# Kernel optimization log

Hardware: AMD Instinct MI355X
Metric: run time of the kernel (lower is better)

Reference implementation:

```python
import jax, jax.numpy as jnp
import numpy as np
from jax import lax

B, C, P = 512, 1, 64
N_MEM = 32768
HID = 16


def _conv(x, w, b):
    # x: [B,Cin,H,W], w: [Cout,Cin,3,3]
    y = lax.conv_general_dilated(x, w, (1, 1), 'SAME',
                                 dimension_numbers=('NCHW', 'OIHW', 'NCHW'))
    return y + b[None, :, None, None]


def setup_inputs() -> dict:
    key = jax.random.key(0)
    ks = jax.random.split(key, 16)
    s = 0.05
    inp = {
        'noisy': jax.random.normal(ks[0], (B, C, P, P), jnp.float32),
        'mem_noise_bank': jax.random.normal(ks[1], (N_MEM, C, P, P), jnp.float32),
        'mem_clean_bank': jax.random.normal(ks[2], (N_MEM, C, P, P), jnp.float32),
        # frozen base denoiser (3-layer residual conv)
        'bw1': jax.random.normal(ks[3], (HID, C, 3, 3), jnp.float32) * s,
        'bb1': jnp.zeros((HID,), jnp.float32),
        'bw2': jax.random.normal(ks[4], (HID, HID, 3, 3), jnp.float32) * s,
        'bb2': jnp.zeros((HID,), jnp.float32),
        'bw3': jax.random.normal(ks[5], (C, HID, 3, 3), jnp.float32) * s,
        'bb3': jnp.zeros((C,), jnp.float32),
        # adapter convs (3*C -> HID -> HID -> C); torch zero-inits last conv,
        # we use small random weights so the output exercises the full path
        'aw1': jax.random.normal(ks[6], (HID, 3 * C, 3, 3), jnp.float32) * s,
        'ab1': jnp.zeros((HID,), jnp.float32),
        'aw2': jax.random.normal(ks[7], (HID, HID, 3, 3), jnp.float32) * s,
        'ab2': jnp.zeros((HID,), jnp.float32),
        'aw3': jax.random.normal(ks[8], (C, HID, 3, 3), jnp.float32) * s,
        'ab3': jnp.zeros((C,), jnp.float32),
    }
    return inp


def _base(noisy, bw1, bb1, bw2, bb2, bw3, bb3):
    h = jax.nn.relu(_conv(noisy, bw1, bb1))
    h = jax.nn.relu(_conv(h, bw2, bb2))
    return noisy - _conv(h, bw3, bb3)


def _select_memory(noisy, mem_noise_bank, mem_clean_bank):
    nf = noisy.reshape(B, -1)                  # [B, D]
    mf = mem_noise_bank.reshape(N_MEM, -1)     # [N, D]
    a2 = jnp.sum(nf * nf, axis=1, keepdims=True)   # [B,1]
    b2 = jnp.sum(mf * mf, axis=1)[None, :]         # [1,N]
    dists = a2 + b2 - 2.0 * (nf @ mf.T)            # [B,N]
    idx = jnp.argmin(dists, axis=1)                # [B]
    return mem_clean_bank[idx]                     # [B,C,P,P]


def reference(noisy, mem_noise_bank, mem_clean_bank,
              bw1, bb1, bw2, bb2, bw3, bb3,
              aw1, ab1, aw2, ab2, aw3, ab3):
    base_out = lax.stop_gradient(_base(noisy, bw1, bb1, bw2, bb2, bw3, bb3))
    mem_clean = lax.stop_gradient(
        _select_memory(noisy, mem_noise_bank, mem_clean_bank))
    x = jnp.concatenate([noisy, base_out, mem_clean], axis=1)  # [B,3C,P,P]
    h = jax.nn.relu(_conv(x, aw1, ab1))
    h = jax.nn.relu(_conv(h, aw2, ab2))
    delta = _conv(h, aw3, ab3)
    return base_out + delta
```

## Files before the change

kernel.cpp:

```cpp
#include <hip/hip_runtime.h>
#include <hip/hip_bf16.h>
#include <cstdint>

#define B_IMG 512
#define NMEM  32768
#define DD    4096
#define HID   16

typedef __attribute__((ext_vector_type(8))) short short8;
typedef __attribute__((ext_vector_type(4))) float f32x4;
typedef unsigned long long ull;

__device__ __forceinline__ void gload16(const void* g, const void* l) {
  __builtin_amdgcn_global_load_lds(
      (const __attribute__((address_space(1))) void*)g,
      (__attribute__((address_space(3))) void*)l, 16, 0, 0);
}

__device__ __forceinline__ ushort to_bf16u(float f) {
  uint32_t u = __float_as_uint(f);
  return (ushort)((u + 0x7fffu + ((u >> 16) & 1u)) >> 16);
}

__device__ __forceinline__ uint32_t cvtpk(float lo, float hi) {
  uint32_t r;
  asm("v_cvt_pk_bf16_f32 %0, %1, %2" : "=v"(r) : "v"(lo), "v"(hi));
  return r;
}

__global__ __launch_bounds__(256) void sqnorm_kernel(const float* __restrict__ x,
                                                     float* __restrict__ out) {
  const int row = blockIdx.x;
  const float4* p = reinterpret_cast<const float4*>(x + (size_t)row * DD);
  float s = 0.f;
#pragma unroll
  for (int j = 0; j < 4; ++j) {
    float4 v = p[threadIdx.x + 256 * j];
    s += v.x * v.x + v.y * v.y + v.z * v.z + v.w * v.w;
  }
#pragma unroll
  for (int o = 32; o > 0; o >>= 1) s += __shfl_down(s, o);
  __shared__ float ls[4];
  if ((threadIdx.x & 63) == 0) ls[threadIdx.x >> 6] = s;
  __syncthreads();
  if (threadIdx.x == 0) out[row] = (ls[0] + ls[1]) + (ls[2] + ls[3]);
}

__global__ __launch_bounds__(256) void split_hi_kernel(const float* __restrict__ x,
                                                       ushort* __restrict__ hi,
                                                       float* __restrict__ nrm) {
  const int row = blockIdx.x;
  const int t = threadIdx.x;
  const float4* p = reinterpret_cast<const float4*>(x + (size_t)row * DD);
  ushort4* ph = reinterpret_cast<ushort4*>(hi + (size_t)row * DD);
  float s = 0.f;
#pragma unroll
  for (int j = 0; j < 4; ++j) {
    float4 v = p[t + 256 * j];
    float vv[4] = {v.x, v.y, v.z, v.w};
    ushort4 h;
    ushort* hp = &h.x;
#pragma unroll
    for (int q = 0; q < 4; ++q) {
      float f = vv[q];
      s += f * f;
      hp[q] = to_bf16u(f);
    }
    ph[t + 256 * j] = h;
  }
#pragma unroll
  for (int o = 32; o > 0; o >>= 1) s += __shfl_down(s, o);
  __shared__ float ls[4];
  if ((t & 63) == 0) ls[t >> 6] = s;
  __syncthreads();
  if (t == 0) nrm[row] = (ls[0] + ls[1]) + (ls[2] + ls[3]);
}

__global__ __launch_bounds__(512) void dist1f_kernel(
    const ushort* __restrict__ Ah_g, const float* __restrict__ Bf,
    const float* __restrict__ a2, float* __restrict__ dists) {
  const int d = blockIdx.x;
  const int xcd = d & 7;
  const int rest = d >> 3;
  const int mb = rest & 3;
  const int nb = (rest >> 2) * 8 + xcd;
  const int m0 = mb * 128;
  const int n0 = nb * 128;

  __shared__ __align__(16) char la[16384];
  __shared__ __align__(16) char lbB[16384];
  __shared__ float b2loc[128];

  const int t = threadIdx.x;
  const int lane = t & 63;
  const int wid = t >> 6;
  const int wm = wid >> 2;
  const int wn = wid & 3;

  f32x4 acc[4][2];
#pragma unroll
  for (int mi = 0; mi < 4; ++mi)
#pragma unroll
    for (int ni = 0; ni < 2; ++ni) {
      f32x4 z = {0.f, 0.f, 0.f, 0.f};
      acc[mi][ni] = z;
    }

  const int r0 = t >> 2, g0 = t & 3;
  const int c0 = ((g0 ^ ((r0 >> 1) & 3)) << 3);
  const float* Bp0 = Bf + (size_t)(n0 + r0) * DD + c0;
  float s0 = 0.f;

  const int arow = t >> 2;
  const int acol = ((g0 ^ ((arow >> 1) & 3)) << 3);

  for (int k0 = 0; k0 < DD; k0 += 64) {
#pragma unroll
    for (int h = 0; h < 2; ++h)
      gload16(Ah_g + ((size_t)(m0 + arow) * DD + k0 + h * 32 + acol),
              la + h * 8192 + t * 16);
#pragma unroll
    for (int h = 0; h < 2; ++h) {
      float4 f00 = *(const float4*)(Bp0 + k0 + h * 32);
      float4 f01 = *(const float4*)(Bp0 + k0 + h * 32 + 4);
      s0 += f00.x * f00.x + f00.y * f00.y + f00.z * f00.z + f00.w * f00.w;
      s0 += f01.x * f01.x + f01.y * f01.y + f01.z * f01.z + f01.w * f01.w;
      uint4 p0;
      p0.x = cvtpk(f00.x, f00.y); p0.y = cvtpk(f00.z, f00.w);
      p0.z = cvtpk(f01.x, f01.y); p0.w = cvtpk(f01.z, f01.w);
      *(uint4*)(lbB + h * 8192 + t * 16) = p0;
    }
    __syncthreads();

#pragma unroll
    for (int h = 0; h < 2; ++h) {
      short8 ah[4];
#pragma unroll
      for (int mi = 0; mi < 4; ++mi) {
        const int r = wm * 64 + mi * 16 + (lane & 15);
        const int off = r * 64 + ((((lane >> 4) ^ (r >> 1)) & 3) << 4);
        ah[mi] = *(const short8*)(la + h * 8192 + off);
      }
#pragma unroll
      for (int ni = 0; ni < 2; ++ni) {
        const int r = wn * 32 + ni * 16 + (lane & 15);
        const int off = r * 64 + ((((lane >> 4) ^ (r >> 1)) & 3) << 4);
        short8 bh = *(const short8*)(lbB + h * 8192 + off);
#pragma unroll
        for (int mi = 0; mi < 4; ++mi)
          acc[mi][ni] = __builtin_amdgcn_mfma_f32_16x16x32_bf16(ah[mi], bh, acc[mi][ni], 0, 0, 0);
      }
    }
    __syncthreads();
  }

  s0 += __shfl_xor(s0, 1); s0 += __shfl_xor(s0, 2);
  if ((t & 3) == 0) b2loc[r0] = s0;
  __syncthreads();

#pragma unroll
  for (int mi = 0; mi < 4; ++mi)
#pragma unroll
    for (int j = 0; j < 4; ++j) {
      const int m = m0 + wm * 64 + mi * 16 + (lane >> 4) * 4 + j;
      const float a2v = a2[m];
#pragma unroll
      for (int ni = 0; ni < 2; ++ni) {
        const int nl = wn * 32 + ni * 16 + (lane & 15);
        dists[(size_t)m * NMEM + n0 + nl] = (a2v + b2loc[nl]) - 2.0f * acc[mi][ni][j];
      }
    }
}

#define MARGIN 4.0f
#define MAXC 64
#define NCH 4
#define CHW (NMEM / NCH)
__global__ __launch_bounds__(256) void refine_kernel(
    const float* __restrict__ dists, const float* __restrict__ A,
    const float* __restrict__ Bm, const float* __restrict__ a2,
    ull* __restrict__ best) {
  const int m = blockIdx.x;
  const int base = blockIdx.y * CHW;
  const int t = threadIdx.x;
  const int lane = t & 63, wid = t >> 6;
  const float4* r4 = reinterpret_cast<const float4*>(dists + (size_t)m * NMEM + base);

  float lmin = 3.4e38f;
  for (int i = t; i < CHW / 4; i += 256) {
    float4 v = r4[i];
    lmin = fminf(lmin, fminf(fminf(v.x, v.y), fminf(v.z, v.w)));
  }
#pragma unroll
  for (int o = 32; o > 0; o >>= 1) lmin = fminf(lmin, __shfl_down(lmin, o));
  __shared__ float ws4[4];
  __shared__ float red[4];
  __shared__ float red2[4];
  __shared__ int cnt;
  __shared__ int cand[MAXC];
  if (lane == 0) ws4[wid] = lmin;
  if (t == 0) cnt = 0;
  __syncthreads();
  const float thresh = fminf(fminf(ws4[0], ws4[1]), fminf(ws4[2], ws4[3])) + MARGIN;

  for (int i = t; i < CHW / 4; i += 256) {
    float4 v = r4[i];
    float vv[4] = {v.x, v.y, v.z, v.w};
#pragma unroll
    for (int q = 0; q < 4; ++q)
      if (vv[q] < thresh) {
        int c = atomicAdd(&cnt, 1);
        if (c < MAXC) cand[c] = base + i * 4 + q;
      }
  }
  __syncthreads();
  const int nc = min(cnt, MAXC);

  ull bkey = ~0ull;
  const float4* a4 = reinterpret_cast<const float4*>(A + (size_t)m * DD);
  for (int c = 0; c < nc; ++c) {
    const int n = cand[c];
    const float4* b4 = reinterpret_cast<const float4*>(Bm + (size_t)n * DD);
    float s = 0.f, s2 = 0.f;
    for (int i = t; i < DD / 4; i += 256) {
      float4 av = a4[i], bv = b4[i];
      s += av.x * bv.x + av.y * bv.y + av.z * bv.z + av.w * bv.w;
      s2 += bv.x * bv.x + bv.y * bv.y + bv.z * bv.z + bv.w * bv.w;
    }
#pragma unroll
    for (int o = 32; o > 0; o >>= 1) {
      s += __shfl_down(s, o);
      s2 += __shfl_down(s2, o);
    }
    if (lane == 0) { red[wid] = s; red2[wid] = s2; }
    __syncthreads();
    if (t == 0) {
      const float dot = (red[0] + red[1]) + (red[2] + red[3]);
      const float b2n = (red2[0] + red2[1]) + (red2[2] + red2[3]);
      const float dv = (a2[m] + b2n) - 2.0f * dot;
      const ull key = ((ull)__float_as_uint(dv) << 32) | (unsigned)n;
      if (key < bkey) bkey = key;
    }
    __syncthreads();
  }
  if (t == 0) atomicMin(&best[m], bkey);
}

__global__ __launch_bounds__(256) void dist_argmin_kernel(
    const float* __restrict__ A, const float* __restrict__ Bm,
    const float* __restrict__ a2, const float* __restrict__ b2,
    ull* __restrict__ best) {
  __shared__ float As[32][128];
  __shared__ float Bs[32][128];
  const int tid = threadIdx.x;
  const int m0 = blockIdx.y * 128;
  const int n0 = blockIdx.x * 128;
  const int tm = tid >> 4, tn = tid & 15;
  const int sr = tid >> 3;
  const int sc = (tid & 7) << 2;
  float acc[8][8];
#pragma unroll
  for (int i = 0; i < 8; ++i)
#pragma unroll
    for (int j = 0; j < 8; ++j) acc[i][j] = 0.f;
  for (int k0 = 0; k0 < DD; k0 += 32) {
    __syncthreads();
#pragma unroll
    for (int r = 0; r < 4; ++r) {
      const int row = sr + (r << 5);
      float4 va = *reinterpret_cast<const float4*>(&A[(size_t)(m0 + row) * DD + k0 + sc]);
      As[sc + 0][row] = va.x; As[sc + 1][row] = va.y;
      As[sc + 2][row] = va.z; As[sc + 3][row] = va.w;
      float4 vb = *reinterpret_cast<const float4*>(&Bm[(size_t)(n0 + row) * DD + k0 + sc]);
      Bs[sc + 0][row] = vb.x; Bs[sc + 1][row] = vb.y;
      Bs[sc + 2][row] = vb.z; Bs[sc + 3][row] = vb.w;
    }
    __syncthreads();
#pragma unroll 8
    for (int kk = 0; kk < 32; ++kk) {
      float4 a0 = *reinterpret_cast<const float4*>(&As[kk][tm * 8]);
      float4 a1 = *reinterpret_cast<const float4*>(&As[kk][tm * 8 + 4]);
      float4 b0 = *reinterpret_cast<const float4*>(&Bs[kk][tn * 8]);
      float4 b1 = *reinterpret_cast<const float4*>(&Bs[kk][tn * 8 + 4]);
      float a[8] = {a0.x, a0.y, a0.z, a0.w, a1.x, a1.y, a1.z, a1.w};
      float b[8] = {b0.x, b0.y, b0.z, b0.w, b1.x, b1.y, b1.z, b1.w};
#pragma unroll
      for (int i = 0; i < 8; ++i)
#pragma unroll
        for (int j = 0; j < 8; ++j) acc[i][j] += a[i] * b[j];
    }
  }
  __syncthreads();
  ull* red = reinterpret_cast<ull*>(&As[0][0]);
#pragma unroll
  for (int i = 0; i < 8; ++i) {
    const int m = m0 + tm * 8 + i;
    const float a2v = a2[m];
    float bd = 3.4e38f;
    int bn = 0;
#pragma unroll
    for (int j = 0; j < 8; ++j) {
      const int n = n0 + tn * 8 + j;
      const float dval = (a2v + b2[n]) - 2.0f * acc[i][j];
      if (dval < bd) { bd = dval; bn = n; }
    }
    red[(tm * 8 + i) * 16 + tn] = ((ull)__float_as_uint(bd) << 32) | (unsigned)bn;
  }
  __syncthreads();
  if (tid < 128) {
    ull k = red[tid * 16];
#pragma unroll
    for (int t2 = 1; t2 < 16; ++t2) {
      ull c = red[tid * 16 + t2];
      if (c < k) k = c;
    }
    atomicMin(&best[m0 + tid], k);
  }
}

__global__ __launch_bounds__(256) void wprep_kernel(
    const float* __restrict__ w1, const float* __restrict__ w2,
    const float* __restrict__ w3, int ncin,
    ushort* __restrict__ wh1, ushort* __restrict__ wl1,
    ushort* __restrict__ wh2, ushort* __restrict__ wl2,
    ushort* __restrict__ wh3, ushort* __restrict__ wl3) {
  const int i = blockIdx.x * 256 + threadIdx.x;
  if (i < 512) {
    const int co = i >> 5, k = i & 31;
    float f = 0.f;
    if (k < ncin * 9) f = w1[(co * ncin + k / 9) * 9 + (k % 9)];
    const ushort hb = to_bf16u(f);
    const float fl = f - __uint_as_float((uint32_t)hb << 16);
    wh1[i] = hb;
    wl1[i] = to_bf16u(fl);
  } else if (i < 512 + 5120) {
    const int j = i - 512;
    const int which = j / 2560;
    const int jj = j % 2560;
    const int co = jj / 160, k = jj % 160;
    float f = 0.f;
    if (which == 0) {
      if (k < 144) f = w2[co * 144 + (k & 15) * 9 + (k >> 4)];
    } else {
      if (co == 0 && k < 144) f = w3[(k & 15) * 9 + (k >> 4)];
    }
    const ushort hb = to_bf16u(f);
    const float fl = f - __uint_as_float((uint32_t)hb << 16);
    ushort* dh = (which == 0) ? wh2 : wh3;
    ushort* dl = (which == 0) ? wl2 : wl3;
    dh[co * 160 + k] = hb;
    dl[co * 160 + k] = to_bf16u(fl);
  }
}

template <int NCIN>
__global__ __launch_bounds__(256, 4) void fused_conv3_kernel(
    const float* __restrict__ chan0, const float* __restrict__ chan1,
    const float* __restrict__ memC, const ull* __restrict__ best,
    const ushort* __restrict__ wh1, const ushort* __restrict__ wl1,
    const float* __restrict__ b1v,
    const ushort* __restrict__ wh2, const ushort* __restrict__ wl2,
    const float* __restrict__ b2v,
    const ushort* __restrict__ wh3, const ushort* __restrict__ wl3,
    const float* __restrict__ b3v,
    const float* __restrict__ addend, float sign, float* __restrict__ outp) {
  constexpr int SIN_SZ = NCIN * 1600;
  constexpr int H1 = SIN_SZ;
  constexpr int H2 = H1 + 10368;
  constexpr int ZP = H2 + 10368;
  constexpr int SB = ZP + 64;
  __shared__ __align__(16) char smem[SB + 128];
  float* sIn = (float*)smem;
  float* sB = (float*)(smem + SB);

  const int tid = threadIdx.x;
  const int lane = tid & 63, wid = tid >> 6;
  const int img = blockIdx.x / 25;
  const int t = blockIdx.x % 25;
  const int y0 = (t / 5) * 14, x0 = (t % 5) * 14;

  const float* cptr[NCIN];
  cptr[0] = chan0 + (size_t)img * DD;
  if (NCIN == 3) {
    cptr[1] = chan1 + (size_t)img * DD;
    cptr[2] = memC + (size_t)(unsigned)(best[img] & 0xffffffffull) * DD;
  }

  if (tid < 16) *(float*)(smem + ZP + tid * 4) = 0.f;
  if (tid < 16) sB[tid] = b1v[tid];
  else if (tid < 32) sB[tid] = b2v[tid - 16];
  for (int i = tid; i < NCIN * 400; i += 256) {
    const int ci = i / 400, r = i % 400, yy = r / 20, xx = r % 20;
    const int gy = y0 + yy - 3, gx = x0 + xx - 3;
    float v = 0.f;
    if (gy >= 0 && gy < 64 && gx >= 0 && gx < 64) v = cptr[ci][gy * 64 + gx];
    sIn[ci * 400 + yy * 20 + xx] = v;
  }
  __syncthreads();

  {
    const int xn15 = lane & 15;
    const int kb = (lane >> 4) * 8;
    const short8 a_hi = *(const short8*)(wh1 + xn15 * 32 + kb);
    const short8 a_lo = *(const short8*)(wl1 + xn15 * 32 + kb);
    int koff[8];
    bool kval[8];
#pragma unroll
    for (int e = 0; e < 8; ++e) {
      const int k = kb + e;
      kval[e] = (k < NCIN * 9);
      const int ci = k / 9, kk = k % 9;
      koff[e] = ci * 400 + (kk / 3) * 20 + (kk % 3);
    }
    for (int g = wid; g < 21; g += 4) {
      const int pxl = g * 16 + xn15;
      const bool pv = (pxl < 324);
      const int py = pxl / 18, pxx = pxl % 18;
      const int pbase = py * 20 + pxx;
      float v[8];
#pragma unroll
      for (int e = 0; e < 8; ++e)
        v[e] = (kval[e] && pv) ? sIn[pbase + koff[e]] : 0.f;
      uint4 bu;
      bu.x = cvtpk(v[0], v[1]); bu.y = cvtpk(v[2], v[3]);
      bu.z = cvtpk(v[4], v[5]); bu.w = cvtpk(v[6], v[7]);
      short8 b = *reinterpret_cast<short8*>(&bu);
      f32x4 z = {0.f, 0.f, 0.f, 0.f};
      f32x4 a1 = __builtin_amdgcn_mfma_f32_16x16x32_bf16(a_lo, b, z, 0, 0, 0);
      a1 = __builtin_amdgcn_mfma_f32_16x16x32_bf16(a_hi, b, a1, 0, 0, 0);
      const int gy = y0 + py - 2, gx = x0 + pxx - 2;
      const bool inimg = pv && ((unsigned)gy < 64u) && ((unsigned)gx < 64u);
      if (pv) {
#pragma unroll
        for (int j = 0; j < 4; ++j) {
          const int co = (lane >> 4) * 4 + j;
          const float val = inimg ? fmaxf(a1[j] + sB[co], 0.f) : 0.f;
          *(ushort*)(smem + H1 + (co >> 3) * 5184 + pxl * 16 + (co & 7) * 2) =
              to_bf16u(val);
        }
      }
    }
  }
  __syncthreads();

  const int xn = lane & 15;
  const int xk = lane >> 4;
  f32x4 acc2[4];
#pragma unroll
  for (int g = 0; g < 4; ++g) { f32x4 z = {0.f, 0.f, 0.f, 0.f}; acc2[g] = z; }
#pragma unroll
  for (int kq = 0; kq < 5; ++kq) {
    const int k0 = kq * 32;
    const int we = xn * 160 + k0 + xk * 8;
    short8 ah = *(const short8*)(wh2 + we);
    short8 al = *(const short8*)(wl2 + we);
    const int kb = k0 + xk * 8;
    const int tap = kb >> 4, cih = (kb >> 3) & 1;
    const bool zp = (tap >= 9);
    const int dy = tap / 3, dx = tap % 3;
    const int bbase = H1 + cih * 5184 + ((dy * 18) + xn + dx) * 16;
#pragma unroll
    for (int g = 0; g < 4; ++g) {
      const int y = wid * 4 + g;
      const int boff = zp ? ZP : (bbase + y * 288);
      short8 b = *(const short8*)(smem + boff);
      acc2[g] = __builtin_amdgcn_mfma_f32_16x16x32_bf16(ah, b, acc2[g], 0, 0, 0);
      acc2[g] = __builtin_amdgcn_mfma_f32_16x16x32_bf16(al, b, acc2[g], 0, 0, 0);
    }
  }
#pragma unroll
  for (int g = 0; g < 4; ++g) {
    const int y = wid * 4 + g;
    const int gy = y0 + y - 1, gx = x0 + xn - 1;
    const bool inimg = ((unsigned)gy < 64u) && ((unsigned)gx < 64u);
#pragma unroll
    for (int j = 0; j < 4; ++j) {
      const int co = xk * 4 + j;
      const float v = inimg ? fmaxf(acc2[g][j] + sB[16 + co], 0.f) : 0.f;
      *(ushort*)(smem + H2 + (co >> 3) * 5184 + (y * 18 + xn) * 16 + (co & 7) * 2) =
          to_bf16u(v);
    }
  }
  __syncthreads();

  f32x4 acc3[4];
#pragma unroll
  for (int g = 0; g < 4; ++g) { f32x4 z = {0.f, 0.f, 0.f, 0.f}; acc3[g] = z; }
#pragma unroll
  for (int kq = 0; kq < 5; ++kq) {
    const int k0 = kq * 32;
    const int we = xn * 160 + k0 + xk * 8;
    short8 ah = *(const short8*)(wh3 + we);
    short8 al = *(const short8*)(wl3 + we);
    const int kb = k0 + xk * 8;
    const int tap = kb >> 4, cih = (kb >> 3) & 1;
    const bool zp = (tap >= 9);
    const int dy = tap / 3, dx = tap % 3;
    const int bbase = H2 + cih * 5184 + ((dy * 18) + xn + dx) * 16;
#pragma unroll
    for (int g = 0; g < 4; ++g) {
      const int y = wid * 4 + g;
      const int boff = zp ? ZP : (bbase + y * 288);
      short8 b = *(const short8*)(smem + boff);
      acc3[g] = __builtin_amdgcn_mfma_f32_16x16x32_bf16(ah, b, acc3[g], 0, 0, 0);
      acc3[g] = __builtin_amdgcn_mfma_f32_16x16x32_bf16(al, b, acc3[g], 0, 0, 0);
    }
  }
  if (xk == 0) {
#pragma unroll
    for (int g = 0; g < 4; ++g) {
      const int y = wid * 4 + g;
      const int gy = y0 + y, gx = x0 + xn;
      if (y < 14 && xn < 14 && gy < 64 && gx < 64) {
        const size_t o = (size_t)img * DD + gy * 64 + gx;
        outp[o] = addend[o] + sign * (acc3[g][0] + b3v[0]);
      }
    }
  }
}

extern "C" void kernel_launch(void* const* d_in, const int* in_sizes, int n_in,
                              void* d_out, int out_size, void* d_ws, size_t ws_size,
                              hipStream_t stream) {
  (void)in_sizes; (void)n_in; (void)out_size;
  const float* noisy = (const float*)d_in[0];
  const float* memN  = (const float*)d_in[1];
  const float* memC  = (const float*)d_in[2];
  const float* bw1 = (const float*)d_in[3];
  const float* bb1 = (const float*)d_in[4];
  const float* bw2 = (const float*)d_in[5];
  const float* bb2 = (const float*)d_in[6];
  const float* bw3 = (const float*)d_in[7];
  const float* bb3 = (const float*)d_in[8];
  const float* aw1 = (const float*)d_in[9];
  const float* ab1 = (const float*)d_in[10];
  const float* aw2 = (const float*)d_in[11];
  const float* ab2 = (const float*)d_in[12];
  const float* aw3 = (const float*)d_in[13];
  const float* ab3 = (const float*)d_in[14];
  float* out_f32 = (float*)d_out;

  char* ws = (char*)d_ws;
  size_t off = 0;
  auto take = [&](size_t bytes) -> char* {
    char* p = ws + off;
    off += (bytes + 255) & ~(size_t)255;
    return p;
  };
  float* b2 = (float*)take((size_t)NMEM * 4);
  float* a2 = (float*)take((size_t)B_IMG * 4);
  ull* best = (ull*)take((size_t)B_IMG * 8);
  float* base_out = (float*)take((size_t)B_IMG * DD * 4);
  ushort* wh1b = (ushort*)take(512 * 2);
  ushort* wl1b = (ushort*)take(512 * 2);
  ushort* wh2b = (ushort*)take(2560 * 2);
  ushort* wl2b = (ushort*)take(2560 * 2);
  ushort* wh3b = (ushort*)take(2560 * 2);
  ushort* wl3b = (ushort*)take(2560 * 2);
  ushort* wh1a = (ushort*)take(512 * 2);
  ushort* wl1a = (ushort*)take(512 * 2);
  ushort* wh2a = (ushort*)take(2560 * 2);
  ushort* wl2a = (ushort*)take(2560 * 2);
  ushort* wh3a = (ushort*)take(2560 * 2);
  ushort* wl3a = (ushort*)take(2560 * 2);
  const size_t off_common = off;

  ushort* Ah = (ushort*)take((size_t)B_IMG * DD * 2);
  float* dists = (float*)take((size_t)B_IMG * NMEM * 4);
  const bool use_mfma = (off + 1024) <= ws_size;
  if (!use_mfma) off = off_common;

  wprep_kernel<<<22, 256, 0, stream>>>(bw1, bw2, bw3, 1, wh1b, wl1b, wh2b, wl2b, wh3b, wl3b);
  wprep_kernel<<<22, 256, 0, stream>>>(aw1, aw2, aw3, 3, wh1a, wl1a, wh2a, wl2a, wh3a, wl3a);

  hipMemsetAsync(best, 0xFF, (size_t)B_IMG * 8, stream);
  if (use_mfma) {
    split_hi_kernel<<<B_IMG, 256, 0, stream>>>(noisy, Ah, a2);
    dist1f_kernel<<<(NMEM / 128) * (B_IMG / 128), 512, 0, stream>>>(
        Ah, memN, a2, dists);
    refine_kernel<<<dim3(B_IMG, NCH), 256, 0, stream>>>(dists, noisy, memN, a2, best);
  } else {
    sqnorm_kernel<<<NMEM, 256, 0, stream>>>(memN, b2);
    sqnorm_kernel<<<B_IMG, 256, 0, stream>>>(noisy, a2);
    dist_argmin_kernel<<<dim3(NMEM / 128, B_IMG / 128), 256, 0, stream>>>(
        noisy, memN, a2, b2, best);
  }

  fused_conv3_kernel<1><<<B_IMG * 25, 256, 0, stream>>>(
      noisy, nullptr, nullptr, nullptr,
      wh1b, wl1b, bb1, wh2b, wl2b, bb2, wh3b, wl3b, bb3, noisy, -1.0f, base_out);
  fused_conv3_kernel<3><<<B_IMG * 25, 256, 0, stream>>>(
      noisy, base_out, memC, best,
      wh1a, wl1a, ab1, wh2a, wl2a, ab2, wh3a, wl3a, ab3, base_out, 1.0f, out_f32);
}
```

Before: 483.9 us.

## Pre-convert memory bank to bf16 and stream both GEMM operands via LDS loads

Adds a separate pass that converts the fp32 memory bank to bf16 and computes its squared norms. The distance GEMM kernel then loads both operands directly into LDS with async global-to-LDS loads, so it no longer does in-loop fp32 loads, conversion and norm accumulation. The GEMM also moves to 256 threads with a 4x4 MFMA tile per wave. The cost is an extra full read of the fp32 bank plus a write and re-read of a 256MB bf16 copy, and a larger workspace that may push the code onto the non-MFMA fallback path.

```diff
diff --git a/kernel.cpp b/kernel.cpp
--- a/kernel.cpp
+++ b/kernel.cpp
@@ -76,9 +76,10 @@
   if (t == 0) nrm[row] = (ls[0] + ls[1]) + (ls[2] + ls[3]);
 }
 
-__global__ __launch_bounds__(512) void dist1f_kernel(
-    const ushort* __restrict__ Ah_g, const float* __restrict__ Bf,
-    const float* __restrict__ a2, float* __restrict__ dists) {
+__global__ __launch_bounds__(256) void dist2_kernel(
+    const ushort* __restrict__ Ah_g, const ushort* __restrict__ Bh_g,
+    const float* __restrict__ a2, const float* __restrict__ b2,
+    float* __restrict__ dists) {
   const int d = blockIdx.x;
   const int xcd = d & 7;
   const int rest = d >> 3;
@@ -88,48 +89,42 @@
   const int n0 = nb * 128;
 
   __shared__ __align__(16) char la[16384];
-  __shared__ __align__(16) char lbB[16384];
-  __shared__ float b2loc[128];
+  __shared__ __align__(16) char lb[16384];
 
   const int t = threadIdx.x;
   const int lane = t & 63;
   const int wid = t >> 6;
-  const int wm = wid >> 2;
-  const int wn = wid & 3;
-
-  f32x4 acc[4][2];
+  const int wm = wid >> 1;
+  const int wn = wid & 1;
+
+  f32x4 acc[4][4];
 #pragma unroll
   for (int mi = 0; mi < 4; ++mi)
 #pragma unroll
-    for (int ni = 0; ni < 2; ++ni) {
+    for (int ni = 0; ni < 4; ++ni) {
       f32x4 z = {0.f, 0.f, 0.f, 0.f};
       acc[mi][ni] = z;
     }
 
-  const int r0 = t >> 2, g0 = t & 3;
-  const int c0 = ((g0 ^ ((r0 >> 1) & 3)) << 3);
-  const float* Bp0 = Bf + (size_t)(n0 + r0) * DD + c0;
-  float s0 = 0.f;
-
-  const int arow = t >> 2;
-  const int acol = ((g0 ^ ((arow >> 1) & 3)) << 3);
+  int arow[2], acol[2];
+#pragma unroll
+  for (int j = 0; j < 2; ++j) {
+    const int e = (j * 256 + t) * 8;
+    arow[j] = e >> 5;
+    const int gpos = (e >> 3) & 3;
+    acol[j] = ((gpos ^ ((arow[j] >> 1) & 3)) << 3);
+  }
 
   for (int k0 = 0; k0 < DD; k0 += 64) {
 #pragma unroll
     for (int h = 0; h < 2; ++h)
-      gload16(Ah_g + ((size_t)(m0 + arow) * DD + k0 + h * 32 + acol),
-              la + h * 8192 + t * 16);
-#pragma unroll
-    for (int h = 0; h < 2; ++h) {
-      float4 f00 = *(const float4*)(Bp0 + k0 + h * 32);
-      float4 f01 = *(const float4*)(Bp0 + k0 + h * 32 + 4);
-      s0 += f00.x * f00.x + f00.y * f00.y + f00.z * f00.z + f00.w * f00.w;
-      s0 += f01.x * f01.x + f01.y * f01.y + f01.z * f01.z + f01.w * f01.w;
-      uint4 p0;
-      p0.x = cvtpk(f00.x, f00.y); p0.y = cvtpk(f00.z, f00.w);
-      p0.z = cvtpk(f01.x, f01.y); p0.w = cvtpk(f01.z, f01.w);
-      *(uint4*)(lbB + h * 8192 + t * 16) = p0;
-    }
+#pragma unroll
+      for (int j = 0; j < 2; ++j) {
+        gload16(Ah_g + ((size_t)(m0 + arow[j]) * DD + k0 + h * 32 + acol[j]),
+                la + h * 8192 + (j * 256 + t) * 16);
+        gload16(Bh_g + ((size_t)(n0 + arow[j]) * DD + k0 + h * 32 + acol[j]),
+                lb + h * 8192 + (j * 256 + t) * 16);
+      }
     __syncthreads();
 
 #pragma unroll
@@ -142,10 +137,10 @@
         ah[mi] = *(const short8*)(la + h * 8192 + off);
       }
 #pragma unroll
-      for (int ni = 0; ni < 2; ++ni) {
-        const int r = wn * 32 + ni * 16 + (lane & 15);
+      for (int ni = 0; ni < 4; ++ni) {
+        const int r = wn * 64 + ni * 16 + (lane & 15);
         const int off = r * 64 + ((((lane >> 4) ^ (r >> 1)) & 3) << 4);
-        short8 bh = *(const short8*)(lbB + h * 8192 + off);
+        short8 bh = *(const short8*)(lb + h * 8192 + off);
 #pragma unroll
         for (int mi = 0; mi < 4; ++mi)
           acc[mi][ni] = __builtin_amdgcn_mfma_f32_16x16x32_bf16(ah[mi], bh, acc[mi][ni], 0, 0, 0);
@@ -153,10 +148,6 @@
     }
     __syncthreads();
   }
-
-  s0 += __shfl_xor(s0, 1); s0 += __shfl_xor(s0, 2);
-  if ((t & 3) == 0) b2loc[r0] = s0;
-  __syncthreads();
 
 #pragma unroll
   for (int mi = 0; mi < 4; ++mi)
@@ -165,9 +156,9 @@
       const int m = m0 + wm * 64 + mi * 16 + (lane >> 4) * 4 + j;
       const float a2v = a2[m];
 #pragma unroll
-      for (int ni = 0; ni < 2; ++ni) {
-        const int nl = wn * 32 + ni * 16 + (lane & 15);
-        dists[(size_t)m * NMEM + n0 + nl] = (a2v + b2loc[nl]) - 2.0f * acc[mi][ni][j];
+      for (int ni = 0; ni < 4; ++ni) {
+        const int n = n0 + wn * 64 + ni * 16 + (lane & 15);
+        dists[(size_t)m * NMEM + n] = (a2v + b2[n]) - 2.0f * acc[mi][ni][j];
       }
     }
 }
@@ -565,6 +556,7 @@
   ushort* wl3a = (ushort*)take(2560 * 2);
   const size_t off_common = off;
 
+  ushort* Bh = (ushort*)take((size_t)NMEM * DD * 2);
   ushort* Ah = (ushort*)take((size_t)B_IMG * DD * 2);
   float* dists = (float*)take((size_t)B_IMG * NMEM * 4);
   const bool use_mfma = (off + 1024) <= ws_size;
@@ -575,9 +567,10 @@
 
   hipMemsetAsync(best, 0xFF, (size_t)B_IMG * 8, stream);
   if (use_mfma) {
+    split_hi_kernel<<<NMEM, 256, 0, stream>>>(memN, Bh, b2);
     split_hi_kernel<<<B_IMG, 256, 0, stream>>>(noisy, Ah, a2);
-    dist1f_kernel<<<(NMEM / 128) * (B_IMG / 128), 512, 0, stream>>>(
-        Ah, memN, a2, dists);
+    dist2_kernel<<<(NMEM / 128) * (B_IMG / 128), 256, 0, stream>>>(
+        Ah, Bh, a2, b2, dists);
     refine_kernel<<<dim3(B_IMG, NCH), 256, 0, stream>>>(dists, noisy, memN, a2, best);
   } else {
     sqnorm_kernel<<<NMEM, 256, 0, stream>>>(memN, b2);
```

After: 591.5 us. 1.22x slower.
